# Kernel tuning notes

Measured on AMD Instinct MI355X. Metric: run time of the kernel, lower is better.

## Reference

```python
import jax, jax.numpy as jnp
import numpy as np

N = 100000   # nodes
E = 3200000  # edges (avg degree 32)
G = 64       # graphs in batch
H = 64       # hidden channels
EPS = 1e-5   # BatchNorm eps


def setup_inputs() -> dict:
    key = jax.random.key(0)
    ks = jax.random.split(key, 32)
    rn = lambda k, s: jax.random.normal(k, s, jnp.float32) * 0.1
    inp = {
        "x": jax.random.normal(ks[0], (N, 3), jnp.float32),
        "edge_index": jax.random.randint(ks[1], (2, E), 0, N),
        "batch": jnp.sort(jax.random.randint(ks[2], (N,), 0, G)),
    }
    dims = [(3, H), (H, H), (H, H)]
    for i, (di, do) in enumerate(dims):
        inp[f"W{i}"] = rn(ks[3 + i], (di, do))
        inp[f"b{i}"] = jnp.zeros((do,), jnp.float32)
        inp[f"g{i}"] = jnp.ones((do,), jnp.float32)
        inp[f"beta{i}"] = jnp.zeros((do,), jnp.float32)
    for j, p in enumerate(["p", "a", "t"]):
        out = 2 if p == "t" else 1
        inp[p + "W1"] = rn(ks[8 + 2 * j], (H, H // 2))
        inp[p + "b1"] = jnp.zeros((H // 2,), jnp.float32)
        inp[p + "W2"] = rn(ks[9 + 2 * j], (H // 2, out))
        inp[p + "b2"] = jnp.zeros((out,), jnp.float32)
    return inp


def _forward(x, edge_index, batch, params):
    (W0, b0, g0, beta0, W1, b1, g1, beta1, W2, b2, g2, beta2,
     pW1, pb1, pW2, pb2, aW1, ab1, aW2, ab2, tW1, tb1, tW2, tb2) = params
    src, dst = edge_index[0], edge_index[1]
    # GCN normalization with self-loops: deg = in-degree + 1
    deg = jax.ops.segment_sum(jnp.ones((E,), x.dtype), dst, num_segments=N) + 1.0
    dis = jax.lax.rsqrt(deg)  # deg^{-1/2}

    def gcn(h_in, W, b):
        h = h_in @ W  # [N, H]
        msg = h[src] * (dis[src] * dis[dst])[:, None]  # [E, H] gather
        out = jax.ops.segment_sum(msg, dst, num_segments=N)  # scatter-add
        out = out + h * (dis * dis)[:, None]  # self-loop term
        return out + b

    def bn_relu(h, g, be):
        m = jnp.mean(h, axis=0)
        v = jnp.var(h, axis=0)  # biased, as torch BN training mode
        return jax.nn.relu(g * (h - m) * jax.lax.rsqrt(v + EPS) + be)

    for W, b, g, be in [(W0, b0, g0, beta0), (W1, b1, g1, beta1), (W2, b2, g2, beta2)]:
        x = bn_relu(gcn(x, W, b), g, be)

    # global_mean_pool over graphs
    counts = jax.ops.segment_sum(jnp.ones((N,), x.dtype), batch, num_segments=G)
    pooled = jax.ops.segment_sum(x, batch, num_segments=G) / jnp.maximum(counts, 1.0)[:, None]

    def head(Wa, ba, Wb, bb):
        return jax.nn.relu(pooled @ Wa + ba) @ Wb + bb

    power = head(pW1, pb1, pW2, pb2)   # [G, 1]
    area = head(aW1, ab1, aW2, ab2)    # [G, 1]
    timing = head(tW1, tb1, tW2, tb2)  # [G, 2] = (tns, wns)
    return jnp.concatenate([power, area, timing], axis=1)  # [G, 4]


def reference(x, edge_index, batch, W0, b0, g0, beta0, W1, b1, g1, beta1,
              W2, b2, g2, beta2, pW1, pb1, pW2, pb2, aW1, ab1, aW2, ab2,
              tW1, tb1, tW2, tb2):
    params = (W0, b0, g0, beta0, W1, b1, g1, beta1, W2, b2, g2, beta2,
              pW1, pb1, pW2, pb2, aW1, ab1, aW2, ab2, tW1, tb1, tW2, tb2)
    return _forward(x, edge_index, batch, params)
```

## Files before the change

### kernel.cpp

```cpp
#include <hip/hip_runtime.h>
#include <hip/hip_fp16.h>

#define EPSBN 1e-5f
#define SH 7
#define CHUNK 16384
#define SCANB 256

__global__ void k_fill(float* __restrict__ p, float v, int n) {
    int i = blockIdx.x * blockDim.x + threadIdx.x;
    if (i < n) p[i] = v;
}

__launch_bounds__(1024)
__global__ void k_hist(const int* __restrict__ dst, int* __restrict__ hist,
                       int E, int C, int NB) {
    __shared__ int h[1024];
    const int tid = threadIdx.x, c = blockIdx.x;
    for (int i = tid; i < NB; i += 1024) h[i] = 0;
    __syncthreads();
    const int e0 = c * CHUNK, e1 = min(e0 + CHUNK, E);
    for (int e = e0 + tid; e < e1; e += 1024) atomicAdd(&h[dst[e] >> SH], 1);
    __syncthreads();
    for (int b = tid; b < NB; b += 1024) hist[b * C + c] = h[b];
}

__launch_bounds__(256)
__global__ void k_scanA(const int* __restrict__ hist, int* __restrict__ bsum, int M) {
    __shared__ int part[256];
    const int b = blockIdx.x, t = threadIdx.x;
    const int seg = (M + SCANB - 1) / SCANB;
    const int lo = b * seg, hi = min(lo + seg, M);
    int s = 0;
    for (int i = lo + t; i < hi; i += 256) s += hist[i];
    part[t] = s;
    __syncthreads();
    for (int d = 128; d > 0; d >>= 1) {
        if (t < d) part[t] += part[t + d];
        __syncthreads();
    }
    if (t == 0) bsum[b] = part[0];
}

__launch_bounds__(256)
__global__ void k_scanB(int* __restrict__ bsum) {
    __shared__ int sh[256];
    const int t = threadIdx.x;
    sh[t] = bsum[t];
    __syncthreads();
    for (int d = 1; d < 256; d <<= 1) {
        int v = (t >= d) ? sh[t - d] : 0;
        __syncthreads();
        sh[t] += v;
        __syncthreads();
    }
    bsum[t] = (t == 0) ? 0 : sh[t - 1];
}

__launch_bounds__(256)
__global__ void k_scanC(int* __restrict__ hist, const int* __restrict__ bsum,
                        int* __restrict__ off, int M, int E, int N) {
    __shared__ int part[256];
    const int b = blockIdx.x, t = threadIdx.x;
    const int seg = (M + SCANB - 1) / SCANB;
    const int lo = b * seg, hi = min(lo + seg, M);
    const int per = (seg + 255) >> 8;
    const int tl = lo + t * per, th = min(tl + per, hi);
    int s = 0;
    for (int i = tl; i < th; ++i) s += hist[i];
    part[t] = s;
    __syncthreads();
    for (int d = 1; d < 256; d <<= 1) {
        int v = (t >= d) ? part[t - d] : 0;
        __syncthreads();
        part[t] += v;
        __syncthreads();
    }
    int run = bsum[b] + ((t == 0) ? 0 : part[t - 1]);
    for (int i = tl; i < th; ++i) {
        int v = hist[i];
        hist[i] = run;
        run += v;
    }
    if (b == 0 && t == 0) off[N] = E;
}

__launch_bounds__(1024)
__global__ void k_sort(const int* __restrict__ src, const int* __restrict__ dst,
                       const int* __restrict__ hist, int2* __restrict__ sorted,
                       int E, int C, int NB) {
    __shared__ int cur[1024];
    const int tid = threadIdx.x, c = blockIdx.x;
    for (int b = tid; b < NB; b += 1024) cur[b] = hist[b * C + c];
    __syncthreads();
    const int e0 = c * CHUNK, e1 = min(e0 + CHUNK, E);
    for (int e = e0 + tid; e < e1; e += 1024) {
        const int d = dst[e];
        const int pos = atomicAdd(&cur[d >> SH], 1);
        sorted[pos] = make_int2(src[e], d);
    }
}

__launch_bounds__(256)
__global__ void k_csr(const int2* __restrict__ sorted, const int* __restrict__ hist,
                      int* __restrict__ off, float* __restrict__ dis,
                      int* __restrict__ eda, int E, int C, int NB, int N) {
    __shared__ int cnt_l[128], scn[128];
    const int tid = threadIdx.x, b = blockIdx.x;
    const int node0 = b << SH;
    const int nloc = min(128, N - node0);
    const int ebeg = hist[b * C];
    const int eend = (b + 1 < NB) ? hist[(b + 1) * C] : E;
    if (tid < 128) cnt_l[tid] = 0;
    __syncthreads();
    for (int e = ebeg + tid; e < eend; e += 256) {
        int2 p = sorted[e];
        atomicAdd(&cnt_l[p.y & 127], 1);
    }
    __syncthreads();
    if (tid < 128) scn[tid] = cnt_l[tid];
    __syncthreads();
    for (int d = 1; d < 128; d <<= 1) {
        int v = 0;
        if (tid < 128 && tid >= d) v = scn[tid - d];
        __syncthreads();
        if (tid < 128) scn[tid] += v;
        __syncthreads();
    }
    if (tid < nloc) {
        const int excl = scn[tid] - cnt_l[tid];
        off[node0 + tid] = ebeg + excl;
        dis[node0 + tid] = rsqrtf((float)cnt_l[tid] + 1.0f);
    }
    __syncthreads();
    if (tid < 128) cnt_l[tid] = scn[tid] - cnt_l[tid];
    __syncthreads();
    for (int e = ebeg + tid; e < eend; e += 256) {
        int2 p = sorted[e];
        const int r = atomicAdd(&cnt_l[p.y & 127], 1);
        eda[ebeg + r] = p.x;
    }
}

template <int K, bool BN>
__launch_bounds__(256)
__global__ void k_linear(const float* __restrict__ X, const float* __restrict__ W,
                         const float* __restrict__ st, const float* __restrict__ g,
                         const float* __restrict__ be, const float* __restrict__ dis,
                         __half* __restrict__ hp, int N) {
    __shared__ float Ws[K * 64];
    __shared__ float Xs[32 * K];
    __shared__ float scs[64], shs[64];
    const int tid = threadIdx.x;
    if (BN && tid < K) {
        const float inv = 1.0f / (float)N;
        const float m = st[tid] * inv;
        const float v = st[64 + tid] * inv - m * m;
        const float sc = g[tid] * rsqrtf(v + EPSBN);
        scs[tid] = sc;
        shs[tid] = fmaf(-m, sc, be[tid]);
    }
    for (int i = tid; i < K * 64; i += 256) Ws[i] = W[i];
    if (BN) __syncthreads();
    const int r0 = blockIdx.x * 32;
    for (int i = tid; i < 32 * K; i += 256) {
        const int r = i / K, c = i - r * K;
        const int row = r0 + r;
        float val = (row < N) ? X[(long)row * K + c] : 0.f;
        if (BN) val = fmaxf(fmaf(val, scs[c], shs[c]), 0.f);
        Xs[i] = val;
    }
    __syncthreads();
    const int c = tid & 63, wv = tid >> 6;
    for (int rr = 0; rr < 8; ++rr) {
        const int r = wv * 8 + rr;
        const int row = r0 + r;
        if (row >= N) break;
        float acc = 0.f;
#pragma unroll
        for (int k = 0; k < K; ++k) acc = fmaf(Xs[r * K + k], Ws[k * 64 + c], acc);
        hp[(long)row * 64 + c] = __float2half(acc * dis[row]);
    }
}

__launch_bounds__(256)
__global__ void k_gather(const int* __restrict__ off, const int* __restrict__ eda,
                         const float* __restrict__ dis, const __half* __restrict__ hp,
                         float* __restrict__ agg, float* __restrict__ st, int N) {
    __shared__ int els[4][64];
    __shared__ float ls[256], ls2[256];
    const int lane = threadIdx.x & 63;
    const int wv = threadIdx.x >> 6;
    const int nwaves = gridDim.x * 4;
    float s = 0.f, s2 = 0.f;
    for (int w = blockIdx.x * 4 + wv; w < N; w += nwaves) {
        const int e0 = off[w], e1 = off[w + 1];
        float acc0 = __half2float(hp[(long)w * 64 + lane]);
        float acc1 = 0.f, acc2 = 0.f, acc3 = 0.f;
        for (int eb = e0; eb < e1; eb += 64) {
            const int mm = min(64, e1 - eb);
            if (eb + lane < e1) els[wv][lane] = eda[eb + lane];
            int j = 0;
            for (; j + 8 <= mm; j += 8) {
                const int s0 = els[wv][j + 0], s1 = els[wv][j + 1];
                const int s2i = els[wv][j + 2], s3 = els[wv][j + 3];
                const int s4 = els[wv][j + 4], s5 = els[wv][j + 5];
                const int s6 = els[wv][j + 6], s7 = els[wv][j + 7];
                const float v0 = __half2float(hp[(long)s0 * 64 + lane]);
                const float v1 = __half2float(hp[(long)s1 * 64 + lane]);
                const float v2 = __half2float(hp[(long)s2i * 64 + lane]);
                const float v3 = __half2float(hp[(long)s3 * 64 + lane]);
                const float v4 = __half2float(hp[(long)s4 * 64 + lane]);
                const float v5 = __half2float(hp[(long)s5 * 64 + lane]);
                const float v6 = __half2float(hp[(long)s6 * 64 + lane]);
                const float v7 = __half2float(hp[(long)s7 * 64 + lane]);
                acc0 += v0 + v4;
                acc1 += v1 + v5;
                acc2 += v2 + v6;
                acc3 += v3 + v7;
            }
            for (; j < mm; ++j) acc0 += __half2float(hp[(long)els[wv][j] * 64 + lane]);
        }
        const float out = dis[w] * ((acc0 + acc1) + (acc2 + acc3));
        agg[(long)w * 64 + lane] = out;
        s += out;
        s2 = fmaf(out, out, s2);
    }
    ls[threadIdx.x] = s;
    ls2[threadIdx.x] = s2;
    __syncthreads();
    if (threadIdx.x < 64) {
        s = ls[lane] + ls[lane + 64] + ls[lane + 128] + ls[lane + 192];
        s2 = ls2[lane] + ls2[lane + 64] + ls2[lane + 128] + ls2[lane + 192];
        unsafeAtomicAdd(&st[lane], s);
        unsafeAtomicAdd(&st[64 + lane], s2);
    }
}

__launch_bounds__(256)
__global__ void k_pool(const float* __restrict__ x, const int* __restrict__ batch,
                       const float* __restrict__ st, const float* __restrict__ g,
                       const float* __restrict__ be, float* __restrict__ poolsum,
                       float* __restrict__ counts, int N, int npw) {
    const int wid = (blockIdx.x * blockDim.x + threadIdx.x) >> 6;
    const int lane = threadIdx.x & 63;
    const int n0 = wid * npw;
    if (n0 >= N) return;
    const float inv = 1.0f / (float)N;
    const float m = st[lane] * inv;
    const float v = st[64 + lane] * inv - m * m;
    const float sc = g[lane] * rsqrtf(v + EPSBN);
    const float sh = fmaf(-m, sc, be[lane]);
    const int n1 = min(n0 + npw, N);
    float acc = 0.f, cnt = 0.f;
    int gr = batch[n0];
    for (int n = n0; n < n1; ++n) {
        int gn = batch[n];
        if (gn != gr) {
            unsafeAtomicAdd(&poolsum[(long)gr * 64 + lane], acc);
            if (lane == 0) unsafeAtomicAdd(&counts[gr], cnt);
            acc = 0.f;
            cnt = 0.f;
            gr = gn;
        }
        acc += fmaxf(fmaf(x[(long)n * 64 + lane], sc, sh), 0.f);
        cnt += 1.f;
    }
    unsafeAtomicAdd(&poolsum[(long)gr * 64 + lane], acc);
    if (lane == 0) unsafeAtomicAdd(&counts[gr], cnt);
}

__launch_bounds__(256)
__global__ void k_heads(const float* __restrict__ poolsum, const float* __restrict__ counts,
                        const float* pW1, const float* pb1, const float* pW2, const float* pb2,
                        const float* aW1, const float* ab1, const float* aW2, const float* ab2,
                        const float* tW1, const float* tb1, const float* tW2, const float* tb2,
                        float* __restrict__ out, int G) {
    __shared__ float P[64 * 64];
    __shared__ float Hd[64 * 32];
    const int tid = threadIdx.x;
    for (int i = tid; i < G * 64; i += 256) {
        int g = i >> 6;
        P[i] = poolsum[i] / fmaxf(counts[g], 1.f);
    }
    __syncthreads();
    for (int j = 0; j < 3; ++j) {
        const float* W1 = (j == 0) ? pW1 : (j == 1) ? aW1 : tW1;
        const float* b1 = (j == 0) ? pb1 : (j == 1) ? ab1 : tb1;
        const float* W2 = (j == 0) ? pW2 : (j == 1) ? aW2 : tW2;
        const float* b2 = (j == 0) ? pb2 : (j == 1) ? ab2 : tb2;
        for (int i = tid; i < G * 32; i += 256) {
            int g = i >> 5, k = i & 31;
            float a = b1[k];
#pragma unroll
            for (int c = 0; c < 64; ++c) a = fmaf(P[g * 64 + c], W1[c * 32 + k], a);
            Hd[i] = fmaxf(a, 0.f);
        }
        __syncthreads();
        const int ow = (j == 2) ? 2 : 1;
        const int off = (j == 2) ? 2 : j;
        for (int i = tid; i < G * ow; i += 256) {
            int g = i / ow, o = i - g * ow;
            float a = b2[o];
#pragma unroll
            for (int k = 0; k < 32; ++k) a = fmaf(Hd[g * 32 + k], W2[k * ow + o], a);
            out[g * 4 + off + o] = a;
        }
        __syncthreads();
    }
}

extern "C" void kernel_launch(void* const* d_in, const int* in_sizes, int n_in,
                              void* d_out, int out_size, void* d_ws, size_t ws_size,
                              hipStream_t stream) {
    const int N = in_sizes[2];
    const int E = in_sizes[1] / 2;
    const int G = out_size / 4;

    const float* x0 = (const float*)d_in[0];
    const int* ei = (const int*)d_in[1];
    const int* src = ei;
    const int* dst = ei + E;
    const int* batch = (const int*)d_in[2];

    const float* W[3] = {(const float*)d_in[3], (const float*)d_in[7], (const float*)d_in[11]};
    const float* gam[3] = {(const float*)d_in[5], (const float*)d_in[9], (const float*)d_in[13]};
    const float* bet[3] = {(const float*)d_in[6], (const float*)d_in[10], (const float*)d_in[14]};

    const float* pW1 = (const float*)d_in[15];
    const float* pb1 = (const float*)d_in[16];
    const float* pW2 = (const float*)d_in[17];
    const float* pb2 = (const float*)d_in[18];
    const float* aW1 = (const float*)d_in[19];
    const float* ab1 = (const float*)d_in[20];
    const float* aW2 = (const float*)d_in[21];
    const float* ab2 = (const float*)d_in[22];
    const float* tW1 = (const float*)d_in[23];
    const float* tb1 = (const float*)d_in[24];
    const float* tW2 = (const float*)d_in[25];
    const float* tb2 = (const float*)d_in[26];

    const int C = (E + CHUNK - 1) / CHUNK;
    const int NB = (N + 127) >> SH;
    const int M = NB * C;

    auto align = [](size_t x) { return (x + 255) & ~(size_t)255; };
    char* w = (char*)d_ws;
    float* dis = (float*)w;      w += align((size_t)N * 4);
    float* bufA = (float*)w;     w += align((size_t)N * 64 * 4);
    __half* hp = (__half*)w;     w += align((size_t)N * 64 * 2);
    float* st = (float*)w;       w += align(3 * 128 * 4);
    float* poolsum = (float*)w;  w += align((size_t)G * 64 * 4);
    float* counts = (float*)w;   w += align((size_t)G * 4);
    int* off = (int*)w;          w += align((size_t)(N + 1) * 4);
    int* hist = (int*)w;         w += align((size_t)M * 4);
    int* bsum = (int*)w;         w += align((size_t)SCANB * 4);
    int2* sorted = (int2*)w;     w += align((size_t)E * 8);
    int* eda = (int*)w;          w += align((size_t)E * 4);
    (void)ws_size;

    const int nb_lin = (N + 31) / 32;
    const int nb_ga = 2048;

    k_hist<<<C, 1024, 0, stream>>>(dst, hist, E, C, NB);
    k_scanA<<<SCANB, 256, 0, stream>>>(hist, bsum, M);
    k_scanB<<<1, 256, 0, stream>>>(bsum);
    k_scanC<<<SCANB, 256, 0, stream>>>(hist, bsum, off, M, E, N);
    k_sort<<<C, 1024, 0, stream>>>(src, dst, hist, sorted, E, C, NB);
    k_csr<<<NB, 256, 0, stream>>>(sorted, hist, off, dis, eda, E, C, NB, N);
    k_fill<<<2, 256, 0, stream>>>(st, 0.f, 3 * 128);

    k_linear<3, false><<<nb_lin, 256, 0, stream>>>(x0, W[0], nullptr, nullptr, nullptr, dis, hp, N);
    k_gather<<<nb_ga, 256, 0, stream>>>(off, eda, dis, hp, bufA, st, N);

    for (int l = 1; l < 3; ++l) {
        k_linear<64, true><<<nb_lin, 256, 0, stream>>>(bufA, W[l], st + (l - 1) * 128,
                                                       gam[l - 1], bet[l - 1], dis, hp, N);
        k_gather<<<nb_ga, 256, 0, stream>>>(off, eda, dis, hp, bufA, st + l * 128, N);
    }

    k_fill<<<(G * 64 + 255) / 256, 256, 0, stream>>>(poolsum, 0.f, G * 64);
    k_fill<<<1, 64, 0, stream>>>(counts, 0.f, G);
    const int npw = 32;
    const int nwaves = (N + npw - 1) / npw;
    const int nb_pool = (nwaves * 64 + 255) / 256;
    k_pool<<<nb_pool, 256, 0, stream>>>(bufA, batch, st + 256, gam[2], bet[2],
                                        poolsum, counts, N, npw);

    k_heads<<<1, 256, 0, stream>>>(poolsum, counts, pW1, pb1, pW2, pb2,
                                   aW1, ab1, aW2, ab2, tW1, tb1, tW2, tb2,
                                   (float*)d_out, G);
}
```

Baseline: 520.2 us.

## Aggregate before transform in first GCN layer, pack sort keys, half2 gather

The first layer now aggregates the 3-wide input features over neighbours (A·X) before multiplying by W0, so the edge gather moves 3 floats per edge instead of 64 halves. A separate small kernel applies W0 and accumulates the BatchNorm statistics, and layer 0 now stays in fp32 rather than going through the fp16 buffer. The sort stage packs the local destination index and the source into one 32-bit word, which halves the traffic of the sorted buffer but assumes N fits in 18 bits. The 64-wide gather reads half2 values, with each half-wave handling alternate edges, and combines the halves with a shuffle.

Measured after the change: 595.6 us. 1.14x slower.

```diff
diff --git a/kernel.cpp b/kernel.cpp
--- a/kernel.cpp
+++ b/kernel.cpp
@@ -86,7 +86,7 @@
 
 __launch_bounds__(1024)
 __global__ void k_sort(const int* __restrict__ src, const int* __restrict__ dst,
-                       const int* __restrict__ hist, int2* __restrict__ sorted,
+                       const int* __restrict__ hist, int* __restrict__ spk,
                        int E, int C, int NB) {
     __shared__ int cur[1024];
     const int tid = threadIdx.x, c = blockIdx.x;
@@ -96,12 +96,12 @@
     for (int e = e0 + tid; e < e1; e += 1024) {
         const int d = dst[e];
         const int pos = atomicAdd(&cur[d >> SH], 1);
-        sorted[pos] = make_int2(src[e], d);
-    }
-}
-
-__launch_bounds__(256)
-__global__ void k_csr(const int2* __restrict__ sorted, const int* __restrict__ hist,
+        spk[pos] = ((d & 127) << 18) | src[e];
+    }
+}
+
+__launch_bounds__(256)
+__global__ void k_csr(const int* __restrict__ spk, const int* __restrict__ hist,
                       int* __restrict__ off, float* __restrict__ dis,
                       int* __restrict__ eda, int E, int C, int NB, int N) {
     __shared__ int cnt_l[128], scn[128];
@@ -113,8 +113,7 @@
     if (tid < 128) cnt_l[tid] = 0;
     __syncthreads();
     for (int e = ebeg + tid; e < eend; e += 256) {
-        int2 p = sorted[e];
-        atomicAdd(&cnt_l[p.y & 127], 1);
+        atomicAdd(&cnt_l[spk[e] >> 18], 1);
     }
     __syncthreads();
     if (tid < 128) scn[tid] = cnt_l[tid];
@@ -135,23 +134,86 @@
     if (tid < 128) cnt_l[tid] = scn[tid] - cnt_l[tid];
     __syncthreads();
     for (int e = ebeg + tid; e < eend; e += 256) {
-        int2 p = sorted[e];
-        const int r = atomicAdd(&cnt_l[p.y & 127], 1);
-        eda[ebeg + r] = p.x;
-    }
-}
-
-template <int K, bool BN>
+        const int p = spk[e];
+        const int r = atomicAdd(&cnt_l[p >> 18], 1);
+        eda[ebeg + r] = p & 0x3FFFF;
+    }
+}
+
+__global__ void k_prex(const float* __restrict__ x0, const float* __restrict__ dis,
+                       float4* __restrict__ x0s4, int N) {
+    int i = blockIdx.x * blockDim.x + threadIdx.x;
+    if (i >= N) return;
+    const float d = dis[i];
+    x0s4[i] = make_float4(d * x0[3 * i], d * x0[3 * i + 1], d * x0[3 * i + 2], 0.f);
+}
+
+__launch_bounds__(256)
+__global__ void k_gather3(const int* __restrict__ off, const int* __restrict__ eda,
+                          const float* __restrict__ dis, const float4* __restrict__ x0s4,
+                          float4* __restrict__ z4, int N) {
+    const int lane = threadIdx.x & 63, wv = threadIdx.x >> 6;
+    const int nw = gridDim.x * 4;
+    for (int w = blockIdx.x * 4 + wv; w < N; w += nw) {
+        const int e0 = off[w], e1 = off[w + 1];
+        float a0 = 0.f, a1 = 0.f, a2 = 0.f;
+        for (int e = e0 + lane; e < e1; e += 64) {
+            float4 v = x0s4[eda[e]];
+            a0 += v.x;
+            a1 += v.y;
+            a2 += v.z;
+        }
+        for (int d = 32; d; d >>= 1) {
+            a0 += __shfl_xor(a0, d);
+            a1 += __shfl_xor(a1, d);
+            a2 += __shfl_xor(a2, d);
+        }
+        if (lane == 0) {
+            const float4 sv = x0s4[w];
+            const float dw = dis[w];
+            z4[w] = make_float4(dw * (a0 + sv.x), dw * (a1 + sv.y), dw * (a2 + sv.z), 0.f);
+        }
+    }
+}
+
+__launch_bounds__(256)
+__global__ void k_lin0(const float4* __restrict__ z4, const float* __restrict__ W,
+                       float* __restrict__ bufA, float* __restrict__ st, int N) {
+    __shared__ float Ws[3 * 64];
+    __shared__ float ls[256], lq[256];
+    const int tid = threadIdx.x;
+    for (int i = tid; i < 192; i += 256) Ws[i] = W[i];
+    __syncthreads();
+    const int c = tid & 63, wv = tid >> 6;
+    float s = 0.f, q = 0.f;
+    for (int r = blockIdx.x * 4 + wv; r < N; r += gridDim.x * 4) {
+        const float4 zr = z4[r];
+        float acc = zr.x * Ws[c] + zr.y * Ws[64 + c] + zr.z * Ws[128 + c];
+        bufA[(long)r * 64 + c] = acc;
+        s += acc;
+        q = fmaf(acc, acc, q);
+    }
+    ls[tid] = s;
+    lq[tid] = q;
+    __syncthreads();
+    if (tid < 64) {
+        s = ls[c] + ls[c + 64] + ls[c + 128] + ls[c + 192];
+        q = lq[c] + lq[c + 64] + lq[c + 128] + lq[c + 192];
+        unsafeAtomicAdd(&st[c], s);
+        unsafeAtomicAdd(&st[64 + c], q);
+    }
+}
+
 __launch_bounds__(256)
 __global__ void k_linear(const float* __restrict__ X, const float* __restrict__ W,
                          const float* __restrict__ st, const float* __restrict__ g,
                          const float* __restrict__ be, const float* __restrict__ dis,
                          __half* __restrict__ hp, int N) {
-    __shared__ float Ws[K * 64];
-    __shared__ float Xs[32 * K];
+    __shared__ float Ws[64 * 64];
+    __shared__ float Xs[32 * 64];
     __shared__ float scs[64], shs[64];
     const int tid = threadIdx.x;
-    if (BN && tid < K) {
+    if (tid < 64) {
         const float inv = 1.0f / (float)N;
         const float m = st[tid] * inv;
         const float v = st[64 + tid] * inv - m * m;
@@ -159,15 +221,14 @@
         scs[tid] = sc;
         shs[tid] = fmaf(-m, sc, be[tid]);
     }
-    for (int i = tid; i < K * 64; i += 256) Ws[i] = W[i];
-    if (BN) __syncthreads();
+    for (int i = tid; i < 64 * 64; i += 256) Ws[i] = W[i];
+    __syncthreads();
     const int r0 = blockIdx.x * 32;
-    for (int i = tid; i < 32 * K; i += 256) {
-        const int r = i / K, c = i - r * K;
+    for (int i = tid; i < 32 * 64; i += 256) {
+        const int r = i >> 6, c = i & 63;
         const int row = r0 + r;
-        float val = (row < N) ? X[(long)row * K + c] : 0.f;
-        if (BN) val = fmaxf(fmaf(val, scs[c], shs[c]), 0.f);
-        Xs[i] = val;
+        float val = (row < N) ? X[(long)row * 64 + c] : 0.f;
+        Xs[i] = fmaxf(fmaf(val, scs[c], shs[c]), 0.f);
     }
     __syncthreads();
     const int c = tid & 63, wv = tid >> 6;
@@ -177,62 +238,88 @@
         if (row >= N) break;
         float acc = 0.f;
 #pragma unroll
-        for (int k = 0; k < K; ++k) acc = fmaf(Xs[r * K + k], Ws[k * 64 + c], acc);
+        for (int k = 0; k < 64; ++k) acc = fmaf(Xs[r * 64 + k], Ws[k * 64 + c], acc);
         hp[(long)row * 64 + c] = __float2half(acc * dis[row]);
     }
 }
 
 __launch_bounds__(256)
-__global__ void k_gather(const int* __restrict__ off, const int* __restrict__ eda,
-                         const float* __restrict__ dis, const __half* __restrict__ hp,
-                         float* __restrict__ agg, float* __restrict__ st, int N) {
+__global__ void k_gather2(const int* __restrict__ off, const int* __restrict__ eda,
+                          const float* __restrict__ dis, const __half2* __restrict__ hp2,
+                          float2* __restrict__ agg2, float* __restrict__ st, int N) {
     __shared__ int els[4][64];
-    __shared__ float ls[256], ls2[256];
+    __shared__ float2 lsum[4][32], lsq[4][32];
     const int lane = threadIdx.x & 63;
     const int wv = threadIdx.x >> 6;
+    const int c2 = lane & 31;
+    const int hi = lane >> 5;
     const int nwaves = gridDim.x * 4;
-    float s = 0.f, s2 = 0.f;
+    float2 sa = {0.f, 0.f}, qa = {0.f, 0.f};
     for (int w = blockIdx.x * 4 + wv; w < N; w += nwaves) {
         const int e0 = off[w], e1 = off[w + 1];
-        float acc0 = __half2float(hp[(long)w * 64 + lane]);
-        float acc1 = 0.f, acc2 = 0.f, acc3 = 0.f;
+        float2 a0 = {0.f, 0.f}, a1 = {0.f, 0.f};
+        {
+            const float2 v = __half22float2(hp2[(long)w * 32 + c2]);
+            if (!hi) a0 = v;
+        }
         for (int eb = e0; eb < e1; eb += 64) {
             const int mm = min(64, e1 - eb);
             if (eb + lane < e1) els[wv][lane] = eda[eb + lane];
             int j = 0;
             for (; j + 8 <= mm; j += 8) {
-                const int s0 = els[wv][j + 0], s1 = els[wv][j + 1];
-                const int s2i = els[wv][j + 2], s3 = els[wv][j + 3];
-                const int s4 = els[wv][j + 4], s5 = els[wv][j + 5];
-                const int s6 = els[wv][j + 6], s7 = els[wv][j + 7];
-                const float v0 = __half2float(hp[(long)s0 * 64 + lane]);
-                const float v1 = __half2float(hp[(long)s1 * 64 + lane]);
-                const float v2 = __half2float(hp[(long)s2i * 64 + lane]);
-                const float v3 = __half2float(hp[(long)s3 * 64 + lane]);
-                const float v4 = __half2float(hp[(long)s4 * 64 + lane]);
-                const float v5 = __half2float(hp[(long)s5 * 64 + lane]);
-                const float v6 = __half2float(hp[(long)s6 * 64 + lane]);
-                const float v7 = __half2float(hp[(long)s7 * 64 + lane]);
-                acc0 += v0 + v4;
-                acc1 += v1 + v5;
-                acc2 += v2 + v6;
-                acc3 += v3 + v7;
+                const int s0 = els[wv][j + hi], s1 = els[wv][j + 2 + hi];
+                const int s2 = els[wv][j + 4 + hi], s3 = els[wv][j + 6 + hi];
+                const float2 v0 = __half22float2(hp2[(long)s0 * 32 + c2]);
+                const float2 v1 = __half22float2(hp2[(long)s1 * 32 + c2]);
+                const float2 v2 = __half22float2(hp2[(long)s2 * 32 + c2]);
+                const float2 v3 = __half22float2(hp2[(long)s3 * 32 + c2]);
+                a0.x += v0.x + v2.x;
+                a0.y += v0.y + v2.y;
+                a1.x += v1.x + v3.x;
+                a1.y += v1.y + v3.y;
             }
-            for (; j < mm; ++j) acc0 += __half2float(hp[(long)els[wv][j] * 64 + lane]);
-        }
-        const float out = dis[w] * ((acc0 + acc1) + (acc2 + acc3));
-        agg[(long)w * 64 + lane] = out;
-        s += out;
-        s2 = fmaf(out, out, s2);
-    }
-    ls[threadIdx.x] = s;
-    ls2[threadIdx.x] = s2;
-    __syncthreads();
-    if (threadIdx.x < 64) {
-        s = ls[lane] + ls[lane + 64] + ls[lane + 128] + ls[lane + 192];
-        s2 = ls2[lane] + ls2[lane + 64] + ls2[lane + 128] + ls2[lane + 192];
-        unsafeAtomicAdd(&st[lane], s);
-        unsafeAtomicAdd(&st[64 + lane], s2);
+            for (; j + 2 <= mm; j += 2) {
+                const int s0 = els[wv][j + hi];
+                const float2 v0 = __half22float2(hp2[(long)s0 * 32 + c2]);
+                a0.x += v0.x;
+                a0.y += v0.y;
+            }
+            if (j < mm && !hi) {
+                const int s0 = els[wv][j];
+                const float2 v0 = __half22float2(hp2[(long)s0 * 32 + c2]);
+                a1.x += v0.x;
+                a1.y += v0.y;
+            }
+        }
+        float ax = a0.x + a1.x, ay = a0.y + a1.y;
+        ax += __shfl_xor(ax, 32);
+        ay += __shfl_xor(ay, 32);
+        const float dw = dis[w];
+        const float2 outv = {dw * ax, dw * ay};
+        if (!hi) agg2[(long)w * 32 + c2] = outv;
+        sa.x += outv.x;
+        sa.y += outv.y;
+        qa.x = fmaf(outv.x, outv.x, qa.x);
+        qa.y = fmaf(outv.y, outv.y, qa.y);
+    }
+    if (!hi) {
+        lsum[wv][c2] = sa;
+        lsq[wv][c2] = qa;
+    }
+    __syncthreads();
+    if (threadIdx.x < 32) {
+        float2 S = {0.f, 0.f}, Q = {0.f, 0.f};
+#pragma unroll
+        for (int k = 0; k < 4; ++k) {
+            S.x += lsum[k][threadIdx.x].x;
+            S.y += lsum[k][threadIdx.x].y;
+            Q.x += lsq[k][threadIdx.x].x;
+            Q.y += lsq[k][threadIdx.x].y;
+        }
+        unsafeAtomicAdd(&st[2 * threadIdx.x], S.x);
+        unsafeAtomicAdd(&st[2 * threadIdx.x + 1], S.y);
+        unsafeAtomicAdd(&st[64 + 2 * threadIdx.x], Q.x);
+        unsafeAtomicAdd(&st[64 + 2 * threadIdx.x + 1], Q.y);
     }
 }
 
@@ -354,10 +441,13 @@
     int* off = (int*)w;          w += align((size_t)(N + 1) * 4);
     int* hist = (int*)w;         w += align((size_t)M * 4);
     int* bsum = (int*)w;         w += align((size_t)SCANB * 4);
-    int2* sorted = (int2*)w;     w += align((size_t)E * 8);
+    int* spk = (int*)w;          w += align((size_t)E * 4);
     int* eda = (int*)w;          w += align((size_t)E * 4);
+    float4* x0s4 = (float4*)w;   w += align((size_t)N * 16);
+    float4* z4 = (float4*)w;     w += align((size_t)N * 16);
     (void)ws_size;
 
+    const int nbN = (N + 255) / 256;
     const int nb_lin = (N + 31) / 32;
     const int nb_ga = 2048;
 
@@ -365,17 +455,19 @@
     k_scanA<<<SCANB, 256, 0, stream>>>(hist, bsum, M);
     k_scanB<<<1, 256, 0, stream>>>(bsum);
     k_scanC<<<SCANB, 256, 0, stream>>>(hist, bsum, off, M, E, N);
-    k_sort<<<C, 1024, 0, stream>>>(src, dst, hist, sorted, E, C, NB);
-    k_csr<<<NB, 256, 0, stream>>>(sorted, hist, off, dis, eda, E, C, NB, N);
+    k_sort<<<C, 1024, 0, stream>>>(src, dst, hist, spk, E, C, NB);
+    k_csr<<<NB, 256, 0, stream>>>(spk, hist, off, dis, eda, E, C, NB, N);
     k_fill<<<2, 256, 0, stream>>>(st, 0.f, 3 * 128);
 
-    k_linear<3, false><<<nb_lin, 256, 0, stream>>>(x0, W[0], nullptr, nullptr, nullptr, dis, hp, N);
-    k_gather<<<nb_ga, 256, 0, stream>>>(off, eda, dis, hp, bufA, st, N);
+    k_prex<<<nbN, 256, 0, stream>>>(x0, dis, x0s4, N);
+    k_gather3<<<512, 256, 0, stream>>>(off, eda, dis, x0s4, z4, N);
+    k_lin0<<<1024, 256, 0, stream>>>(z4, W[0], bufA, st, N);
 
     for (int l = 1; l < 3; ++l) {
-        k_linear<64, true><<<nb_lin, 256, 0, stream>>>(bufA, W[l], st + (l - 1) * 128,
-                                                       gam[l - 1], bet[l - 1], dis, hp, N);
-        k_gather<<<nb_ga, 256, 0, stream>>>(off, eda, dis, hp, bufA, st + l * 128, N);
+        k_linear<<<nb_lin, 256, 0, stream>>>(bufA, W[l], st + (l - 1) * 128,
+                                             gam[l - 1], bet[l - 1], dis, hp, N);
+        k_gather2<<<nb_ga, 256, 0, stream>>>(off, eda, dis, (const __half2*)hp,
+                                             (float2*)bufA, st + l * 128, N);
     }
 
     k_fill<<<(G * 64 + 255) / 256, 256, 0, stream>>>(poolsum, 0.f, G * 64);
```
